# Optimization experiments

Measured on AMD Instinct MI355X. Metric: run time of the kernel, lower is better.

## Reference

```python
import jax, jax.numpy as jnp
import numpy as np

B, S, D, H, DH = 4, 2048, 512, 8, 64  # batch, seq, input_dim, heads, per-head output_dim


def setup_inputs() -> dict:
    key = jax.random.key(0)
    ks = jax.random.split(key, 10)
    scale = 0.02
    inp = {
        "x": jax.random.normal(ks[0], (B, S, D), dtype=jnp.float32),
        "biological_mask": jnp.ones((B, S), dtype=bool),
        "Wq": jax.random.normal(ks[1], (D, H * DH), dtype=jnp.float32) * scale,
        "bq": jnp.zeros((H * DH,), dtype=jnp.float32),
        "Wk": jax.random.normal(ks[2], (D, H * DH), dtype=jnp.float32) * scale,
        "bk": jnp.zeros((H * DH,), dtype=jnp.float32),
        "Wv": jax.random.normal(ks[3], (D, H * DH), dtype=jnp.float32) * scale,
        "bv": jnp.zeros((H * DH,), dtype=jnp.float32),
        "Wo": jax.random.normal(ks[4], (H * DH, DH), dtype=jnp.float32) * scale,
        "bo": jnp.zeros((DH,), dtype=jnp.float32),
        "prior_weight": jnp.full((1,), 0.1, dtype=jnp.float32),
    }
    return inp


def reference(x, biological_mask, Wq, bq, Wk, bk, Wv, bv, Wo, bo, prior_weight):
    b, s, _ = x.shape
    inv_sqrt_dh = jnp.float32(1.0 / np.sqrt(DH))
    # projections -> [B,H,S,DH]
    q = (x @ Wq + bq).reshape(b, s, H, DH).transpose(0, 2, 1, 3)
    k = (x @ Wk + bk).reshape(b, s, H, DH).transpose(0, 2, 1, 3)
    v = (x @ Wv + bv).reshape(b, s, H, DH).transpose(0, 2, 1, 3)
    # scores [B,H,S,S]
    scores = jnp.einsum("bhqd,bhkd->bhqk", q, k) * inv_sqrt_dh
    # biological prior: identity matrix, broadcast over batch and heads
    prior = jnp.eye(s, dtype=scores.dtype)[None, None, :, :]
    scores = scores + prior_weight[0] * prior
    attn = jax.nn.softmax(scores, axis=-1)  # dropout is identity in eval mode
    attended = jnp.einsum("bhqk,bhkd->bhqd", attn, v)
    attended = attended.transpose(0, 2, 1, 3).reshape(b, s, H * DH)
    return attended @ Wo + bo
```

## Files before the change

kernel.cpp:

```cpp
#include <hip/hip_runtime.h>
#include <hip/hip_bf16.h>

#define B_ 4
#define S_ 2048
#define D_ 512
#define H_ 8
#define DH_ 64
#define HD_ 512
#define M_ 8192
#define QKVN 1536
#define QKN 1024
#define LOG2E 1.4426950408889634f

typedef __attribute__((ext_vector_type(8))) short bf16x8;
typedef __attribute__((ext_vector_type(4))) float f32x4;
typedef unsigned short u16;

__device__ inline u16 f2bf(float f) {
    __hip_bfloat16 h = __float2bfloat16(f);
    return *reinterpret_cast<u16*>(&h);
}

__device__ inline void async_cp16(const void* g, void* l) {
    __builtin_amdgcn_global_load_lds(
        (const __attribute__((address_space(1))) unsigned int*)g,
        (__attribute__((address_space(3))) unsigned int*)l, 16, 0, 0);
}

__global__ __launch_bounds__(256) void prep_all(
    const float* __restrict__ x, const float* __restrict__ Wq,
    const float* __restrict__ Wk, const float* __restrict__ Wv,
    const float* __restrict__ Wo, u16* __restrict__ xb,
    u16* __restrict__ WqkvT, u16* __restrict__ WoT)
{
    const int z = blockIdx.z;
    const int tid = threadIdx.x;

    if (z == 4) {
        const int id = blockIdx.y * 64 + blockIdx.x;
#pragma unroll
        for (int it = 0; it < 4; ++it) {
            int i = it * 131072 + id * 256 + tid;
            float4 a = *reinterpret_cast<const float4*>(&x[(size_t)i * 8]);
            float4 b = *reinterpret_cast<const float4*>(&x[(size_t)i * 8 + 4]);
            bf16x8 o;
            o[0] = f2bf(a.x); o[1] = f2bf(a.y); o[2] = f2bf(a.z); o[3] = f2bf(a.w);
            o[4] = f2bf(b.x); o[5] = f2bf(b.y); o[6] = f2bf(b.z); o[7] = f2bf(b.w);
            *reinterpret_cast<bf16x8*>(&xb[(size_t)i * 8]) = o;
        }
        return;
    }

    const float* src; u16* dst; int R, C;
    if (z < 3) { if (blockIdx.x >= 8) return;
                 src = (z == 0) ? Wq : (z == 1) ? Wk : Wv;
                 dst = WqkvT + (size_t)z * 512 * 512; R = 512; C = 512; }
    else       { if (blockIdx.x) return; src = Wo; dst = WoT; R = 512; C = 64; }

    __shared__ u16 T[64][65];
    const int c0 = blockIdx.x * 64, r0 = blockIdx.y * 64;
#pragma unroll
    for (int i = 0; i < 4; ++i) {
        int idx = i * 256 + tid;
        int r = idx >> 4, q4 = (idx & 15) << 2;
        float4 vv = *reinterpret_cast<const float4*>(&src[(size_t)(r0 + r) * C + c0 + q4]);
        T[r][q4 + 0] = f2bf(vv.x); T[r][q4 + 1] = f2bf(vv.y);
        T[r][q4 + 2] = f2bf(vv.z); T[r][q4 + 3] = f2bf(vv.w);
    }
    __syncthreads();
#pragma unroll
    for (int i = 0; i < 2; ++i) {
        int idx = i * 256 + tid;
        int cc = idx >> 3, jj = idx & 7;
        bf16x8 o;
#pragma unroll
        for (int e = 0; e < 8; ++e) o[e] = (short)T[jj * 8 + e][cc];
        *reinterpret_cast<bf16x8*>(&dst[(size_t)(c0 + cc) * R + r0 + jj * 8]) = o;
    }
}

__global__ __launch_bounds__(256) void gemm_qkv(
    const u16* __restrict__ A, const u16* __restrict__ BT,
    const float* __restrict__ bq, const float* __restrict__ bk,
    const float* __restrict__ bv, u16* __restrict__ qk,
    u16* __restrict__ vT, float qscale)
{
    __shared__ __align__(16) u16 As[128 * 64];
    __shared__ __align__(16) u16 Bs[128 * 64];
    const int tid = threadIdx.x, lane = tid & 63, w = tid >> 6;
    const int l15 = lane & 15, l4 = lane >> 4;

    const int bidf = blockIdx.x;
    const int xcd = bidf & 7, pos = bidf >> 3;
    const int swz = xcd * 96 + pos;
    const int by = swz / 12, bx = swz - by * 12;
    const int tm = by * 128, tn = bx * 128;
    const int wm = (w >> 1) * 64, wn = (w & 1) * 64;

    f32x4 acc[4][4] = {};

    for (int k0 = 0; k0 < 512; k0 += 64) {
#pragma unroll
        for (int i = 0; i < 4; ++i) {
            int call = w * 4 + i;
            int c = call * 64 + lane;
            int r = c >> 3, j = c & 7;
            async_cp16(A + (size_t)(tm + r) * 512 + k0 + ((j ^ (r & 7)) << 3),
                       &As[call * 512]);
            async_cp16(BT + (size_t)(tn + r) * 512 + k0 + ((j ^ (r & 7)) << 3),
                       &Bs[call * 512]);
        }
        __syncthreads();
#pragma unroll
        for (int ks = 0; ks < 2; ++ks) {
            bf16x8 af[4], bf[4];
#pragma unroll
            for (int mf = 0; mf < 4; ++mf) {
                int r = wm + mf * 16 + l15;
                int j = ks * 4 + l4;
                af[mf] = *reinterpret_cast<const bf16x8*>(&As[(r * 8 + (j ^ (r & 7))) * 8]);
            }
#pragma unroll
            for (int nf = 0; nf < 4; ++nf) {
                int r = wn + nf * 16 + l15;
                int j = ks * 4 + l4;
                bf[nf] = *reinterpret_cast<const bf16x8*>(&Bs[(r * 8 + (j ^ (r & 7))) * 8]);
            }
#pragma unroll
            for (int mf = 0; mf < 4; ++mf)
#pragma unroll
                for (int nf = 0; nf < 4; ++nf)
                    acc[mf][nf] = __builtin_amdgcn_mfma_f32_16x16x32_bf16(
                        af[mf], bf[nf], acc[mf][nf], 0, 0, 0);
        }
        __syncthreads();
    }
#pragma unroll
    for (int nf = 0; nf < 4; ++nf) {
        const int col = tn + wn + nf * 16 + l15;
        if (col < QKN) {
            const float bias_v = (col < 512) ? bq[col] : bk[col - 512];
            const float scl = (col < 512) ? qscale : 1.0f;
#pragma unroll
            for (int mf = 0; mf < 4; ++mf)
#pragma unroll
                for (int r = 0; r < 4; ++r) {
                    int row = tm + wm + mf * 16 + l4 * 4 + r;
                    qk[(size_t)row * QKN + col] = f2bf((acc[mf][nf][r] + bias_v) * scl);
                }
        } else {
            const int dcol = col - QKN;
            const float bias_v = bv[dcol];
            const int hh = dcol >> 6, dd = dcol & 63;
#pragma unroll
            for (int mf = 0; mf < 4; ++mf) {
                int row0 = tm + wm + mf * 16 + l4 * 4;
                int bb = row0 >> 11, s0 = row0 & 2047;
                ushort4 pk;
                pk.x = f2bf(acc[mf][nf][0] + bias_v);
                pk.y = f2bf(acc[mf][nf][1] + bias_v);
                pk.z = f2bf(acc[mf][nf][2] + bias_v);
                pk.w = f2bf(acc[mf][nf][3] + bias_v);
                *reinterpret_cast<ushort4*>(
                    &vT[((size_t)(bb * 8 + hh) * 64 + dd) * S_ + s0]) = pk;
            }
        }
    }
}

__global__ __launch_bounds__(256, 4) void flash_mfma(
    const u16* __restrict__ qk, const u16* __restrict__ vT,
    const float* __restrict__ pw_ptr, u16* __restrict__ att)
{
    __shared__ __align__(16) u16 Kb[2][4096];
    __shared__ __align__(16) u16 Vb[2][4096];

    const int tid = threadIdx.x, lane = tid & 63, w = tid >> 6;
    const int l15 = lane & 15, l4 = lane >> 4;
    const int bid = blockIdx.x;
    const int x = bid & 7, g = bid >> 3;
    const int bh = x * 4 + (g >> 5), qt = g & 31;
    const int h = bh & 7, b = bh >> 3;
    const float pwl = pw_ptr[0] * LOG2E;

    const u16* qbase = qk + (size_t)b * S_ * QKN + h * 64;
    const u16* kbase = qbase + 512;
    const u16* vtb   = vT + (size_t)bh * DH_ * S_;

    const int qrow0 = qt * 64 + w * 16;
    bf16x8 qb[2];
#pragma unroll
    for (int ks2 = 0; ks2 < 2; ++ks2)
        qb[ks2] = *reinterpret_cast<const bf16x8*>(
            &qbase[(size_t)(qrow0 + l15) * QKN + ks2 * 32 + l4 * 8]);

    const bf16x8 ones = {(short)0x3F80, (short)0x3F80, (short)0x3F80, (short)0x3F80,
                         (short)0x3F80, (short)0x3F80, (short)0x3F80, (short)0x3F80};

    f32x4 accv[4] = {};
    f32x4 accl = {};
    const int diag_t = qt;

#define STAGE(buf, jj) do {                                                        \
    _Pragma("unroll")                                                              \
    for (int i_ = 0; i_ < 2; ++i_) {                                               \
        int call_ = w * 2 + i_;                                                    \
        int c_ = call_ * 64 + lane;                                                \
        int rho_ = c_ >> 3, j_ = c_ & 7;                                           \
        int pi_ = (rho_ & 32) | ((rho_ & 12) << 1) | ((rho_ & 16) >> 2)            \
                | (rho_ & 3);                                                      \
        async_cp16(kbase + (size_t)((jj) + pi_) * QKN + ((j_ ^ (rho_ & 7)) << 3),  \
                   &Kb[buf][call_ * 512]);                                         \
        async_cp16(vtb + (size_t)rho_ * S_ + (jj) + ((j_ ^ (rho_ & 7)) << 3),      \
                   &Vb[buf][call_ * 512]);                                         \
    } } while (0)

    STAGE(0, 0);
    __syncthreads();
    int cur = 0;

    for (int t = 0; t < 32; ++t) {
        const int j0 = t << 6;
        if (t < 31) STAGE(cur ^ 1, j0 + 64);

        f32x4 s[4] = {};
        __builtin_amdgcn_s_setprio(1);
#pragma unroll
        for (int c = 0; c < 4; ++c)
#pragma unroll
            for (int ks2 = 0; ks2 < 2; ++ks2) {
                const int rr = c * 16 + l15;
                const int sl = ks2 * 4 + l4;
                bf16x8 ka = *reinterpret_cast<const bf16x8*>(
                    &Kb[cur][(rr * 8 + (sl ^ (rr & 7))) * 8]);
                s[c] = __builtin_amdgcn_mfma_f32_16x16x32_bf16(ka, qb[ks2], s[c], 0, 0, 0);
            }
        __builtin_amdgcn_s_setprio(0);

        if (t == diag_t) {
#pragma unroll
            for (int c = 0; c < 4; ++c)
#pragma unroll
                for (int r = 0; r < 4; ++r) {
                    int kv = (c >> 1) * 32 + l4 * 8 + (c & 1) * 4 + r;
                    if (j0 + kv == qrow0 + l15) s[c][r] += pwl;
                }
        }

        bf16x8 pa[2];
#pragma unroll
        for (int ks = 0; ks < 2; ++ks)
#pragma unroll
            for (int d2 = 0; d2 < 2; ++d2)
#pragma unroll
                for (int r = 0; r < 4; ++r)
                    pa[ks][d2 * 4 + r] = (short)f2bf(exp2f(s[ks * 2 + d2][r]));

        __builtin_amdgcn_s_setprio(1);
        accl = __builtin_amdgcn_mfma_f32_16x16x32_bf16(pa[0], ones, accl, 0, 0, 0);
        accl = __builtin_amdgcn_mfma_f32_16x16x32_bf16(pa[1], ones, accl, 0, 0, 0);
#pragma unroll
        for (int nf = 0; nf < 4; ++nf) {
            const int d = nf * 16 + l15;
#pragma unroll
            for (int ks = 0; ks < 2; ++ks) {
                const int sl = ks * 4 + l4;
                bf16x8 vb = *reinterpret_cast<const bf16x8*>(
                    &Vb[cur][(d * 8 + (sl ^ (d & 7))) * 8]);
                accv[nf] = __builtin_amdgcn_mfma_f32_16x16x32_bf16(pa[ks], vb, accv[nf], 0, 0, 0);
            }
        }
        __builtin_amdgcn_s_setprio(0);

        __syncthreads();
        cur ^= 1;
    }
#undef STAGE

#pragma unroll
    for (int r = 0; r < 4; ++r) {
        float inv = 1.0f / accl[r];
        int row = qrow0 + l4 * 4 + r;
#pragma unroll
        for (int nf = 0; nf < 4; ++nf)
            att[(size_t)(b * S_ + row) * HD_ + h * 64 + nf * 16 + l15] =
                f2bf(accv[nf][r] * inv);
    }
}

__global__ __launch_bounds__(64) void out_proj(
    const u16* __restrict__ att, const u16* __restrict__ WoT,
    const float* __restrict__ bo, float* __restrict__ out)
{
    const int lane = threadIdx.x;
    const int l15 = lane & 15, l4 = lane >> 4;
    const int row0 = blockIdx.x * 16;

    f32x4 acc[4] = {};
#pragma unroll 4
    for (int ks = 0; ks < 16; ++ks) {
        bf16x8 a = *reinterpret_cast<const bf16x8*>(
            &att[(size_t)(row0 + l15) * 512 + ks * 32 + l4 * 8]);
#pragma unroll
        for (int nf = 0; nf < 4; ++nf) {
            bf16x8 bb = *reinterpret_cast<const bf16x8*>(
                &WoT[(size_t)(nf * 16 + l15) * 512 + ks * 32 + l4 * 8]);
            acc[nf] = __builtin_amdgcn_mfma_f32_16x16x32_bf16(a, bb, acc[nf], 0, 0, 0);
        }
    }
#pragma unroll
    for (int nf = 0; nf < 4; ++nf) {
        int n = nf * 16 + l15;
        float bias_v = bo[n];
#pragma unroll
        for (int r = 0; r < 4; ++r)
            out[(size_t)(row0 + l4 * 4 + r) * 64 + n] = acc[nf][r] + bias_v;
    }
}

extern "C" void kernel_launch(void* const* d_in, const int* in_sizes, int n_in,
                              void* d_out, int out_size, void* d_ws, size_t ws_size,
                              hipStream_t stream)
{
    const float* x  = (const float*)d_in[0];
    const float* Wq = (const float*)d_in[2];
    const float* bq = (const float*)d_in[3];
    const float* Wk = (const float*)d_in[4];
    const float* bk = (const float*)d_in[5];
    const float* Wv = (const float*)d_in[6];
    const float* bv = (const float*)d_in[7];
    const float* Wo = (const float*)d_in[8];
    const float* bo = (const float*)d_in[9];
    const float* pw = (const float*)d_in[10];

    u16* ws = (u16*)d_ws;
    size_t o = 0;
    u16* xb    = ws + o; o += (size_t)M_ * D_;
    u16* WqkvT = ws + o; o += (size_t)QKVN * D_;
    u16* WoT   = ws + o; o += (size_t)DH_ * HD_;
    u16* qkb   = ws + o; o += (size_t)M_ * QKN;
    u16* vTt   = ws + o; o += (size_t)M_ * HD_;
    u16* att   = ws + o; o += (size_t)M_ * HD_;

    dim3 blk(256);
    prep_all<<<dim3(64, 8, 5), blk, 0, stream>>>(x, Wq, Wk, Wv, Wo, xb, WqkvT, WoT);

    gemm_qkv<<<dim3(768), blk, 0, stream>>>(
        xb, WqkvT, bq, bk, bv, qkb, vTt, 0.125f * LOG2E);

    flash_mfma<<<dim3(1024), blk, 0, stream>>>(qkb, vTt, pw, att);

    out_proj<<<dim3(M_ / 16), dim3(64), 0, stream>>>(att, WoT, bo, (float*)d_out);
}
```

Measured before the change: 104.7 us.

## Store V pre-swizzled in MFMA fragment order and load it directly from global

The QKV GEMM now writes V into a layout that matches the MFMA B-operand fragment order per key tile. The flash kernel drops the LDS staging of V and has each lane load its fragments straight from global (L2) memory, split into two batches around the QK^T compute. This is meant to halve the LDS traffic and shared memory per block. The cost is that every wave (four per block) re-reads the same V tile from global/L2 instead of sharing one LDS copy, and the load latency is exposed inside the loop.

```diff
diff --git a/kernel.cpp b/kernel.cpp
--- a/kernel.cpp
+++ b/kernel.cpp
@@ -83,7 +83,7 @@
     const u16* __restrict__ A, const u16* __restrict__ BT,
     const float* __restrict__ bq, const float* __restrict__ bk,
     const float* __restrict__ bv, u16* __restrict__ qk,
-    u16* __restrict__ vT, float qscale)
+    u16* __restrict__ v3, float qscale)
 {
     __shared__ __align__(16) u16 As[128 * 64];
     __shared__ __align__(16) u16 Bs[128 * 64];
@@ -151,29 +151,32 @@
         } else {
             const int dcol = col - QKN;
             const float bias_v = bv[dcol];
-            const int hh = dcol >> 6, dd = dcol & 63;
+            const int hh = dcol >> 6, d64 = dcol & 63;
+            const int n = d64 >> 4, dd = d64 & 15;
 #pragma unroll
             for (int mf = 0; mf < 4; ++mf) {
                 int row0 = tm + wm + mf * 16 + l4 * 4;
-                int bb = row0 >> 11, s0 = row0 & 2047;
+                int b = row0 >> 11, s = row0 & 2047;
+                int t = s >> 6, s6 = s & 63;
+                int ks = s6 >> 5, l4i = (s6 >> 3) & 3, kvi = s6 & 7;
                 ushort4 pk;
                 pk.x = f2bf(acc[mf][nf][0] + bias_v);
                 pk.y = f2bf(acc[mf][nf][1] + bias_v);
                 pk.z = f2bf(acc[mf][nf][2] + bias_v);
                 pk.w = f2bf(acc[mf][nf][3] + bias_v);
-                *reinterpret_cast<ushort4*>(
-                    &vT[((size_t)(bb * 8 + hh) * 64 + dd) * S_ + s0]) = pk;
+                size_t idx = (((((size_t)(b * 8 + hh) * 32 + t) * 4 + n) * 2 + ks) * 4
+                              + l4i) * 128 + dd * 8 + kvi;
+                *reinterpret_cast<ushort4*>(&v3[idx]) = pk;
             }
         }
     }
 }
 
 __global__ __launch_bounds__(256, 4) void flash_mfma(
-    const u16* __restrict__ qk, const u16* __restrict__ vT,
+    const u16* __restrict__ qk, const u16* __restrict__ v3,
     const float* __restrict__ pw_ptr, u16* __restrict__ att)
 {
     __shared__ __align__(16) u16 Kb[2][4096];
-    __shared__ __align__(16) u16 Vb[2][4096];
 
     const int tid = threadIdx.x, lane = tid & 63, w = tid >> 6;
     const int l15 = lane & 15, l4 = lane >> 4;
@@ -185,7 +188,7 @@
 
     const u16* qbase = qk + (size_t)b * S_ * QKN + h * 64;
     const u16* kbase = qbase + 512;
-    const u16* vtb   = vT + (size_t)bh * DH_ * S_;
+    const u16* vbase = v3 + (size_t)bh * 32 * 4 * 2 * 512 + l4 * 128 + l15 * 8;
 
     const int qrow0 = qt * 64 + w * 16;
     bf16x8 qb[2];
@@ -211,8 +214,6 @@
                 | (rho_ & 3);                                                      \
         async_cp16(kbase + (size_t)((jj) + pi_) * QKN + ((j_ ^ (rho_ & 7)) << 3),  \
                    &Kb[buf][call_ * 512]);                                         \
-        async_cp16(vtb + (size_t)rho_ * S_ + (jj) + ((j_ ^ (rho_ & 7)) << 3),      \
-                   &Vb[buf][call_ * 512]);                                         \
     } } while (0)
 
     STAGE(0, 0);
@@ -221,6 +222,16 @@
 
     for (int t = 0; t < 32; ++t) {
         const int j0 = t << 6;
+        const u16* vt = vbase + (size_t)t * 4096;
+
+        bf16x8 vb01[2][2];
+#pragma unroll
+        for (int n = 0; n < 2; ++n)
+#pragma unroll
+            for (int ks = 0; ks < 2; ++ks)
+                vb01[n][ks] = *reinterpret_cast<const bf16x8*>(
+                    vt + (n * 2 + ks) * 512);
+
         if (t < 31) STAGE(cur ^ 1, j0 + 64);
 
         f32x4 s[4] = {};
@@ -237,6 +248,14 @@
             }
         __builtin_amdgcn_s_setprio(0);
 
+        bf16x8 vb23[2][2];
+#pragma unroll
+        for (int n = 0; n < 2; ++n)
+#pragma unroll
+            for (int ks = 0; ks < 2; ++ks)
+                vb23[n][ks] = *reinterpret_cast<const bf16x8*>(
+                    vt + ((n + 2) * 2 + ks) * 512);
+
         if (t == diag_t) {
 #pragma unroll
             for (int c = 0; c < 4; ++c)
@@ -260,16 +279,17 @@
         accl = __builtin_amdgcn_mfma_f32_16x16x32_bf16(pa[0], ones, accl, 0, 0, 0);
         accl = __builtin_amdgcn_mfma_f32_16x16x32_bf16(pa[1], ones, accl, 0, 0, 0);
 #pragma unroll
-        for (int nf = 0; nf < 4; ++nf) {
-            const int d = nf * 16 + l15;
-#pragma unroll
-            for (int ks = 0; ks < 2; ++ks) {
-                const int sl = ks * 4 + l4;
-                bf16x8 vb = *reinterpret_cast<const bf16x8*>(
-                    &Vb[cur][(d * 8 + (sl ^ (d & 7))) * 8]);
-                accv[nf] = __builtin_amdgcn_mfma_f32_16x16x32_bf16(pa[ks], vb, accv[nf], 0, 0, 0);
-            }
-        }
+        for (int n = 0; n < 2; ++n)
+#pragma unroll
+            for (int ks = 0; ks < 2; ++ks)
+                accv[n] = __builtin_amdgcn_mfma_f32_16x16x32_bf16(
+                    pa[ks], vb01[n][ks], accv[n], 0, 0, 0);
+#pragma unroll
+        for (int n = 0; n < 2; ++n)
+#pragma unroll
+            for (int ks = 0; ks < 2; ++ks)
+                accv[n + 2] = __builtin_amdgcn_mfma_f32_16x16x32_bf16(
+                    pa[ks], vb23[n][ks], accv[n + 2], 0, 0, 0);
         __builtin_amdgcn_s_setprio(0);
 
         __syncthreads();
@@ -339,16 +359,16 @@
     u16* WqkvT = ws + o; o += (size_t)QKVN * D_;
     u16* WoT   = ws + o; o += (size_t)DH_ * HD_;
     u16* qkb   = ws + o; o += (size_t)M_ * QKN;
-    u16* vTt   = ws + o; o += (size_t)M_ * HD_;
+    u16* v3b   = ws + o; o += (size_t)M_ * HD_;
     u16* att   = ws + o; o += (size_t)M_ * HD_;
 
     dim3 blk(256);
     prep_all<<<dim3(64, 8, 5), blk, 0, stream>>>(x, Wq, Wk, Wv, Wo, xb, WqkvT, WoT);
 
     gemm_qkv<<<dim3(768), blk, 0, stream>>>(
-        xb, WqkvT, bq, bk, bv, qkb, vTt, 0.125f * LOG2E);
-
-    flash_mfma<<<dim3(1024), blk, 0, stream>>>(qkb, vTt, pw, att);
+        xb, WqkvT, bq, bk, bv, qkb, v3b, 0.125f * LOG2E);
+
+    flash_mfma<<<dim3(1024), blk, 0, stream>>>(qkb, v3b, pw, att);
 
     out_proj<<<dim3(M_ / 16), dim3(64), 0, stream>>>(att, WoT, bo, (float*)d_out);
 }
```

Result: faster. 99.68 us (-4.8%).
